# Kernel optimization log

Measured on AMD Instinct MI355X. Metric: run time of the kernel, lower is better.

The kernel has to match this reference:

```python
import jax, jax.numpy as jnp
import numpy as np

D = 128          # embed_features
N = 4096         # cells per batch
M = 8192         # genes / regions
FB1, FB2, FR, FA = 100, 100, 256, 512


def setup_inputs() -> dict:
    key = jax.random.key(0)
    ks = jax.random.split(key, 16)
    s = 0.05  # weight scale to keep activations in a sane range
    return {
        "u1": jax.random.normal(ks[0], (N, FB1), jnp.float32),
        "u2": jax.random.normal(ks[1], (N, FB2), jnp.float32),
        "v1": jax.random.normal(ks[2], (M, FR), jnp.float32),
        "v2": jax.random.normal(ks[3], (M, FA), jnp.float32),
        # linear layers stored as [in, out] so y = x @ W
        "Wb1": jax.random.normal(ks[4], (FB1, D), jnp.float32) * s,
        "Wb2": jax.random.normal(ks[5], (FB2, D), jnp.float32) * s,
        "Wrna1": jax.random.normal(ks[6], (FR, 2 * D), jnp.float32) * s,
        "Wrna2": jax.random.normal(ks[7], (2 * D, D), jnp.float32) * s,
        "gene_act": jax.random.normal(ks[8], (FA, FR), jnp.float32) * s,
        "w_prod1": jax.random.normal(ks[9], (D,), jnp.float32),
        "w_add1": jax.random.normal(ks[10], (2 * D,), jnp.float32),
        "w_prod2": jax.random.normal(ks[11], (D,), jnp.float32),
        "w_add2": jax.random.normal(ks[12], (2 * D,), jnp.float32),
        "bias_1": jax.random.normal(ks[13], (), jnp.float32),
        "bias_2": jax.random.normal(ks[14], (), jnp.float32),
    }


def _pair_scores(eu, ev, w_prod, w_add, bias):
    # Algebraically identical to the original all-pairs form:
    #   (eu[:,None,:] * ev[None,:,:]) @ w_prod  ==  (eu * w_prod) @ ev.T
    #   cat(eu, ev) @ w_add  ==  eu @ w_add[:D]  +  ev @ w_add[D:]
    prod = (eu * w_prod) @ ev.T                     # [N, M]
    add = (eu @ w_add[:D])[:, None] + (ev @ w_add[D:])[None, :]
    return prod + add + bias                        # [N, M]


def reference(u1, u2, v1, v2, Wb1, Wb2, Wrna1, Wrna2, gene_act,
              w_prod1, w_add1, w_prod2, w_add2, bias_1, bias_2):
    # mode='linear' activations -> identity
    embed_u1 = u1 @ Wb1                                          # [N, D]
    embed_v1 = jax.nn.relu(v1 @ Wrna1) @ Wrna2                   # [M, D]
    out1 = jax.nn.relu(_pair_scores(embed_u1, embed_v1, w_prod1, w_add1, bias_1))

    embed_u2 = u2 @ Wb2                                          # [N, D]
    embed_v2 = jax.nn.relu((v2 @ gene_act) @ Wrna1) @ Wrna2      # [M, D]
    out2 = jax.nn.sigmoid(_pair_scores(embed_u2, embed_v2, w_prod2, w_add2, bias_2))

    return out1, out2, embed_u1, embed_v1, embed_u2, embed_v2
```

## Files before the change

### kernel.cpp

```cpp
#include <hip/hip_runtime.h>
#include <math.h>

#define N_CELLS 4096
#define M_GENES 8192

typedef __attribute__((ext_vector_type(8))) short short8;
typedef __attribute__((ext_vector_type(4))) float f32x4;

__device__ __align__(16) float g_a[24576];

__device__ __align__(16) short g_bu1[N_CELLS * 128];
__device__ __align__(16) short g_bv1[M_GENES * 128];
__device__ __align__(16) short g_bu2[N_CELLS * 128];
__device__ __align__(16) short g_bv2[M_GENES * 128];

__device__ __align__(16) short g_gaT[256 * 512];
__device__ __align__(16) short g_W1T[256 * 256];
__device__ __align__(16) short g_W2T[128 * 256];


__device__ __forceinline__ short* bf_sel(int s) {
    switch (s) {
        case 0:  return g_bu1;
        case 1:  return g_bv1;
        case 2:  return g_bu2;
        default: return g_bv2;
    }
}

__device__ __forceinline__ const short* wt_sel(int s) {
    switch (s) {
        case 0:  return g_gaT;
        case 1:  return g_W1T;
        default: return g_W2T;
    }
}

__device__ __forceinline__ short f2bf(float f) {
    unsigned u = __builtin_bit_cast(unsigned, f);
    u += 0x7FFFu + ((u >> 16) & 1u);
    return (short)(u >> 16);
}

__device__ __forceinline__ void cvt8(const float* __restrict__ in, short* __restrict__ out) {
    const float4 x0 = *reinterpret_cast<const float4*>(in);
    const float4 x1 = *reinterpret_cast<const float4*>(in + 4);
    short8 o;
    o[0] = f2bf(x0.x); o[1] = f2bf(x0.y); o[2] = f2bf(x0.z); o[3] = f2bf(x0.w);
    o[4] = f2bf(x1.x); o[5] = f2bf(x1.y); o[6] = f2bf(x1.z); o[7] = f2bf(x1.w);
    *reinterpret_cast<short8*>(out) = o;
}

__device__ __forceinline__ void transpose8(const float* __restrict__ in, short* __restrict__ out,
                                           int c, int K, int Nc) {
    const int o0 = c * 8;
    const int ncol = o0 / K;
    const int k0 = o0 % K;
    short8 o;
#pragma unroll
    for (int j = 0; j < 8; ++j) o[j] = f2bf(in[(size_t)(k0 + j) * Nc + ncol]);
    *reinterpret_cast<short8*>(out + o0) = o;
}

__device__ __forceinline__ void stage_A_f32(char* cA, const float* Af, int row0, int k0, int K, int t)
{
    const float* gAf = Af + (size_t)row0 * K + k0;
#pragma unroll
    for (int c = 0; c < 4; ++c) {
        const int idx = c * 256 + t;
        const int row = idx >> 4, sub = idx & 15;
        const int dst = row * 256 + ((sub * 16) ^ ((row & 7) << 4));
        cvt8(gAf + (size_t)row * K + sub * 8, (short*)(cA + dst));
    }
}

__device__ __forceinline__ void stage_B128(char* cB, const short* BT, int col0, int k0, int K, int t)
{
    const char* gB = (const char*)(BT + (size_t)col0 * K + k0);
#pragma unroll
    for (int c = 0; c < 8; ++c) {
        const int idx = c * 256 + t;
        const int row = idx >> 4, sub = idx & 15;
        const int dst = row * 256 + ((sub * 16) ^ ((row & 7) << 4));
        *(short8*)(cB + dst) = *(const short8*)(gB + (size_t)row * (2 * K) + sub * 16);
    }
}

__device__ __forceinline__ void stage_B64(char* cB, const short* BT, int col0, int k0, int K, int t)
{
    const char* gB = (const char*)(BT + (size_t)col0 * K + k0);
#pragma unroll
    for (int c = 0; c < 4; ++c) {
        const int idx = c * 256 + t;
        const int row = idx >> 4, sub = idx & 15;
        const int dst = row * 256 + ((sub * 16) ^ ((row & 7) << 4));
        *(short8*)(cB + dst) = *(const short8*)(gB + (size_t)row * (2 * K) + sub * 16);
    }
}

__device__ __forceinline__ void mfma128(const char* cA, int strideA, int baseA,
                                        const char* cB, f32x4 (&acc)[2][4], int t)
{
    const int l = t & 63, w = t >> 6;
    const int wm = (w >> 1) * 32, wn = (w & 1) * 64;
    const int lr = l & 15, lkb = (l >> 4) * 16;
#pragma unroll
    for (int kk = 0; kk < 4; ++kk) {
        const int kb = kk * 64 + lkb;
        short8 a[2], b4[4];
#pragma unroll
        for (int i = 0; i < 2; ++i) {
            const int rA = wm + i * 16 + lr;
            a[i] = *(const short8*)(cA + rA * strideA + ((baseA + kb) ^ ((rA & 7) << 4)));
        }
#pragma unroll
        for (int jj = 0; jj < 4; ++jj) {
            const int rB = wn + jj * 16 + lr;
            b4[jj] = *(const short8*)(cB + rB * 256 + (kb ^ ((rB & 7) << 4)));
        }
#pragma unroll
        for (int i = 0; i < 2; ++i)
#pragma unroll
            for (int jj = 0; jj < 4; ++jj)
                acc[i][jj] = __builtin_amdgcn_mfma_f32_16x16x32_bf16(a[i], b4[jj], acc[i][jj], 0, 0, 0);
    }
}

__device__ __forceinline__ void mfma64(const char* cA, int strideA, int baseA,
                                       const char* cB, f32x4 (&acc)[4], int t)
{
    const int l = t & 63, w = t >> 6;
    const int wm = w * 16;
    const int lr = l & 15, lkb = (l >> 4) * 16;
#pragma unroll
    for (int kk = 0; kk < 4; ++kk) {
        const int kb = kk * 64 + lkb;
        const int rA = wm + lr;
        const short8 a = *(const short8*)(cA + rA * strideA + ((baseA + kb) ^ ((rA & 7) << 4)));
#pragma unroll
        for (int jj = 0; jj < 4; ++jj) {
            const int rB = jj * 16 + lr;
            const short8 b = *(const short8*)(cB + rB * 256 + (kb ^ ((rB & 7) << 4)));
            acc[jj] = __builtin_amdgcn_mfma_f32_16x16x32_bf16(a, b, acc[jj], 0, 0, 0);
        }
    }
}

__device__ __forceinline__ void acc_to_sH(char* sH, const f32x4 (&acc)[2][4], int ct, bool relu, int t)
{
    const int l = t & 63, w = t >> 6;
    const int wm = (w >> 1) * 32, wn = (w & 1) * 64;
    const int lr = l & 15, r4 = (l >> 4) * 4;
#pragma unroll
    for (int i = 0; i < 2; ++i)
#pragma unroll
        for (int r = 0; r < 4; ++r) {
            const int row = wm + i * 16 + r4 + r;
#pragma unroll
            for (int jj = 0; jj < 4; ++jj) {
                float x = acc[i][jj][r];
                if (relu) x = fmaxf(x, 0.f);
                const int col = ct * 128 + wn + jj * 16 + lr;
                *(short*)(sH + row * 512 + ((col * 2) ^ ((row & 7) << 4))) = f2bf(x);
            }
        }
}

__device__ __forceinline__ void acc2_to_sH(char* sH, const f32x4 (&a4)[4], int ct, bool relu, int t)
{
    const int l = t & 63, w = t >> 6;
    const int lr = l & 15, r4 = (l >> 4) * 4;
#pragma unroll
    for (int r = 0; r < 4; ++r) {
        const int row = w * 16 + r4 + r;
#pragma unroll
        for (int jj = 0; jj < 4; ++jj) {
            float x = a4[jj][r];
            if (relu) x = fmaxf(x, 0.f);
            const int col = ct * 64 + jj * 16 + lr;
            *(short*)(sH + row * 512 + ((col * 2) ^ ((row & 7) << 4))) = f2bf(x);
        }
    }
}

__device__ __forceinline__ void first_layer(const float* Vf, int row0, int KV, int bsel, bool relu,
                                            char* cA, char* cH, int t)
{
    const short* BT = wt_sel(bsel);
    f32x4 accA[2][4] = {}, accB[2][4] = {};
    for (int k0 = 0; k0 < KV; k0 += 128) {
        stage_A_f32(cA, Vf, row0, k0, KV, t);
        stage_B128(cH, BT, 0, k0, KV, t);
        __syncthreads();
        mfma128(cA, 256, 0, cH, accA, t);
        __syncthreads();
        stage_B128(cH, BT, 128, k0, KV, t);
        __syncthreads();
        mfma128(cA, 256, 0, cH, accB, t);
        __syncthreads();
    }
    acc_to_sH(cH, accA, 0, relu, t);
    acc_to_sH(cH, accB, 1, relu, t);
    __syncthreads();
}

__device__ __forceinline__ void mid_layer(char* cH, char* cB64, int t)
{
    const short* W1T = wt_sel(1);
    f32x4 h4[4][4];
#pragma unroll
    for (int ct = 0; ct < 4; ++ct)
#pragma unroll
        for (int jj = 0; jj < 4; ++jj) h4[ct][jj] = (f32x4){0.f, 0.f, 0.f, 0.f};
#pragma unroll
    for (int ct = 0; ct < 4; ++ct)
        for (int k0 = 0; k0 < 2; ++k0) {
            stage_B64(cB64, W1T, ct * 64, k0 * 128, 256, t);
            __syncthreads();
            mfma64(cH, 512, k0 * 256, cB64, h4[ct], t);
            __syncthreads();
        }
#pragma unroll
    for (int ct = 0; ct < 4; ++ct) acc2_to_sH(cH, h4[ct], ct, true, t);
    __syncthreads();
}

__device__ __forceinline__ void final_layer(char* cH, char* cB64, float* evout, short* bv,
                                            const float* w_add_hi, int a_ofs, int row0, int t)
{
    const short* W2T = wt_sel(2);
    const int l = t & 63, w = t >> 6, lr = l & 15, r4 = (l >> 4) * 4;
    float part[4] = {0.f, 0.f, 0.f, 0.f};
#pragma unroll
    for (int ct = 0; ct < 2; ++ct) {
        f32x4 a2[4] = {};
        for (int k0 = 0; k0 < 2; ++k0) {
            stage_B64(cB64, W2T, ct * 64, k0 * 128, 256, t);
            __syncthreads();
            mfma64(cH, 512, k0 * 256, cB64, a2, t);
            __syncthreads();
        }
#pragma unroll
        for (int r = 0; r < 4; ++r) {
            const int grow = row0 + w * 16 + r4 + r;
#pragma unroll
            for (int jj = 0; jj < 4; ++jj) {
                const float x = a2[jj][r];
                const int col = ct * 64 + jj * 16 + lr;
                evout[(size_t)grow * 128 + col] = x;
                bv[(size_t)grow * 128 + col] = f2bf(x);
                part[r] = fmaf(x, w_add_hi[col], part[r]);
            }
        }
    }
#pragma unroll
    for (int off = 1; off < 16; off <<= 1)
#pragma unroll
        for (int r = 0; r < 4; ++r) part[r] += __shfl_xor(part[r], off, 64);
    if (lr == 0) {
#pragma unroll
        for (int r = 0; r < 4; ++r) g_a[a_ofs + row0 + w * 16 + r4 + r] = part[r];
    }
}

__device__ __forceinline__ void embed8(int be, const float* u1, const float* u2,
        const float* Wb1, const float* Wb2, const float* wp1, const float* wa1,
        const float* wp2, const float* wa2, float* eu1, float* eu2, float* sMemF)
{
    const int which = (be >= 512) ? 1 : 0;
    const int bl = which ? (be - 512) : be;
    const float* u  = which ? u2 : u1;
    const float* Wb = which ? Wb2 : Wb1;
    const float* wp = which ? wp2 : wp1;
    const float* wa = which ? wa2 : wa1;
    float* e  = which ? eu2 : eu1;
    short* bu = bf_sel(which ? 2 : 0);
    const int a_ofs = which ? 12288 : 0;
    const int row0 = bl * 8;
    float* sWb = sMemF;
    float* sUu = sMemF + 12800;
    float* sF  = sMemF + 13600;
    const int t = threadIdx.x;
    for (int c = t; c < 3200; c += 256)
        ((float4*)sWb)[c] = ((const float4*)Wb)[c];
    for (int c = t; c < 800; c += 256) sUu[c] = u[row0 * 100 + c];
    if (t < 8) sF[t] = 0.f;
    __syncthreads();
    const int d = t & 127, g = t >> 7;
    float acc[4] = {0.f, 0.f, 0.f, 0.f};
    for (int k = 0; k < 100; ++k) {
        const float wv = sWb[k * 128 + d];
#pragma unroll
        for (int rr = 0; rr < 4; ++rr) acc[rr] = fmaf(wv, sUu[(g * 4 + rr) * 100 + k], acc[rr]);
    }
    const float wpd = wp[d], wad = wa[d];
    float pv[4];
#pragma unroll
    for (int rr = 0; rr < 4; ++rr) {
        const int row = row0 + g * 4 + rr;
        e[(size_t)row * 128 + d] = acc[rr];
        bu[(size_t)row * 128 + d] = f2bf(acc[rr] * wpd);
        pv[rr] = acc[rr] * wad;
    }
#pragma unroll
    for (int off = 32; off > 0; off >>= 1)
#pragma unroll
        for (int rr = 0; rr < 4; ++rr) pv[rr] += __shfl_down(pv[rr], off, 64);
    if ((t & 63) == 0) {
#pragma unroll
        for (int rr = 0; rr < 4; ++rr) atomicAdd(&sF[g * 4 + rr], pv[rr]);
    }
    __syncthreads();
    if (t < 8) g_a[a_ofs + row0 + t] = sF[t];
}

__global__ __launch_bounds__(256) void prep_w(const float* __restrict__ gene_act,
                                              const float* __restrict__ W1,
                                              const float* __restrict__ W2)
{
    const int b = blockIdx.x, t = threadIdx.x;
    if (b < 64)      transpose8(gene_act, g_gaT, b * 256 + t, 512, 256);
    else if (b < 96) transpose8(W1, g_W1T, (b - 64) * 256 + t, 256, 256);
    else             transpose8(W2, g_W2T, (b - 96) * 256 + t, 256, 128);
}

__global__ __launch_bounds__(256) void fused_mid(const float* __restrict__ v1,
                                                 const float* __restrict__ v2,
                                                 const float* __restrict__ u1,
                                                 const float* __restrict__ u2,
                                                 const float* __restrict__ Wb1,
                                                 const float* __restrict__ Wb2,
                                                 const float* __restrict__ wp1,
                                                 const float* __restrict__ wa1,
                                                 const float* __restrict__ wp2,
                                                 const float* __restrict__ wa2,
                                                 float* __restrict__ eu1,
                                                 float* __restrict__ eu2,
                                                 float* __restrict__ ev1,
                                                 float* __restrict__ ev2)
{
    __shared__ __align__(16) short sMem[32768];
    char* cA   = (char*)sMem;
    char* cB64 = cA + 16384;
    char* cH   = cA + 32768;
    const int b = blockIdx.x, t = threadIdx.x;
    if (b < 128) {
        const int row0 = b * 64;
        first_layer(v2, row0, 512, 0, false, cA, cH, t);
        mid_layer(cH, cB64, t);
        final_layer(cH, cB64, ev2, bf_sel(3), wa2 + 128, 16384, row0, t);
    } else if (b < 256) {
        const int row0 = (b - 128) * 64;
        first_layer(v1, row0, 256, 1, true, cA, cH, t);
        final_layer(cH, cB64, ev1, bf_sel(1), wa1 + 128, 4096, row0, t);
    } else {
        embed8(b - 256, u1, u2, Wb1, Wb2, wp1, wa1, wp2, wa2, eu1, eu2, (float*)sMem);
    }
}

__global__ __launch_bounds__(256) void pair_both(const float* __restrict__ bias1,
                                                 const float* __restrict__ bias2,
                                                 float* __restrict__ out1,
                                                 float* __restrict__ out2)
{
    __shared__ __align__(16) short sA[128 * 128];
    __shared__ __align__(16) short sB[128 * 128];
    const int which = blockIdx.z;
    const int t = threadIdx.x;
    const int l = t & 63;
    const int row0 = blockIdx.y * 128;
    const int col0 = blockIdx.x * 128;

    {
        const short8* gA = reinterpret_cast<const short8*>(bf_sel(which ? 2 : 0)) + (size_t)row0 * 16;
        const short8* gB = reinterpret_cast<const short8*>(bf_sel(which ? 3 : 1)) + (size_t)col0 * 16;
        char* cA = (char*)sA;
        char* cB = (char*)sB;
#pragma unroll
        for (int c = 0; c < 8; ++c) {
            const int idx = c * 256 + t;
            const int row = idx >> 4, sub = idx & 15;
            const int dst = row * 256 + ((sub * 16) ^ ((row & 7) << 4));
            const short8 va = gA[idx];
            const short8 vb = gB[idx];
            *(short8*)(cA + dst) = va;
            *(short8*)(cB + dst) = vb;
        }
    }
    __syncthreads();

    const int w  = t >> 6;
    const int wm = (w >> 1) * 64;
    const int wn = (w & 1) * 64;
    const int lr = l & 15;
    const int lkb = (l >> 4) * 16;

    f32x4 acc[4][4] = {};
    const char* cA = (const char*)sA;
    const char* cB = (const char*)sB;
#pragma unroll
    for (int kk = 0; kk < 4; ++kk) {
        const int kb = kk * 64 + lkb;
        short8 a[4], bfr[4];
#pragma unroll
        for (int i = 0; i < 4; ++i) {
            const int rowA = wm + i * 16 + lr;
            a[i] = *(const short8*)(cA + rowA * 256 + (kb ^ ((rowA & 7) << 4)));
            const int rowB = wn + i * 16 + lr;
            bfr[i] = *(const short8*)(cB + rowB * 256 + (kb ^ ((rowB & 7) << 4)));
        }
#pragma unroll
        for (int i = 0; i < 4; ++i)
#pragma unroll
            for (int jj = 0; jj < 4; ++jj)
                acc[i][jj] = __builtin_amdgcn_mfma_f32_16x16x32_bf16(a[i], bfr[jj], acc[i][jj], 0, 0, 0);
    }

    const float bias = which ? *bias2 : *bias1;
    float* outp = which ? out2 : out1;
    const int ofsU = which ? 12288 : 0;
    const int ofsV = which ? 16384 : 4096;
    const int r4 = (l >> 4) * 4;
    float au[4][4];
#pragma unroll
    for (int i = 0; i < 4; ++i)
#pragma unroll
        for (int r = 0; r < 4; ++r)
            au[i][r] = g_a[ofsU + row0 + wm + i * 16 + r4 + r];
    float av[4];
#pragma unroll
    for (int jj = 0; jj < 4; ++jj)
        av[jj] = g_a[ofsV + col0 + wn + jj * 16 + lr];

#pragma unroll
    for (int i = 0; i < 4; ++i) {
#pragma unroll
        for (int r = 0; r < 4; ++r) {
            const int grow = row0 + wm + i * 16 + r4 + r;
            float* orow = outp + (size_t)grow * M_GENES + col0 + wn;
#pragma unroll
            for (int jj = 0; jj < 4; ++jj) {
                float x = acc[i][jj][r] + au[i][r] + av[jj] + bias;
                if (which == 0) x = fmaxf(x, 0.f);
                else            x = __builtin_amdgcn_rcpf(1.f + __expf(-x));
                orow[jj * 16 + lr] = x;
            }
        }
    }
}

extern "C" void kernel_launch(void* const* d_in, const int* in_sizes, int n_in,
                              void* d_out, int out_size, void* d_ws, size_t ws_size,
                              hipStream_t stream)
{
    const float* u1       = (const float*)d_in[0];
    const float* u2       = (const float*)d_in[1];
    const float* v1       = (const float*)d_in[2];
    const float* v2       = (const float*)d_in[3];
    const float* Wb1      = (const float*)d_in[4];
    const float* Wb2      = (const float*)d_in[5];
    const float* Wrna1    = (const float*)d_in[6];
    const float* Wrna2    = (const float*)d_in[7];
    const float* gene_act = (const float*)d_in[8];
    const float* w_prod1  = (const float*)d_in[9];
    const float* w_add1   = (const float*)d_in[10];
    const float* w_prod2  = (const float*)d_in[11];
    const float* w_add2   = (const float*)d_in[12];
    const float* bias1    = (const float*)d_in[13];
    const float* bias2    = (const float*)d_in[14];

    float* out  = (float*)d_out;
    float* out1 = out;
    float* out2 = out1 + (size_t)N_CELLS * M_GENES;
    float* eu1  = out2 + (size_t)N_CELLS * M_GENES;
    float* ev1  = eu1 + N_CELLS * 128;
    float* eu2  = ev1 + M_GENES * 128;
    float* ev2  = eu2 + N_CELLS * 128;

    prep_w<<<112, 256, 0, stream>>>(gene_act, Wrna1, Wrna2);

    fused_mid<<<1280, 256, 0, stream>>>(v1, v2, u1, u2, Wb1, Wb2,
                                        w_prod1, w_add1, w_prod2, w_add2,
                                        eu1, eu2, ev1, ev2);

    pair_both<<<dim3(64, 32, 2), 256, 0, stream>>>(bias1, bias2, out1, out2);
}
```

Baseline: 114.7 us.

## Stage pair-score outputs through LDS for coalesced float4 stores, use 512 threads

The pair kernel now runs 512 threads per block with 8 waves each computing a 64x32 sub-tile, which halves the per-wave accumulators and raises wave count. The output tile is written into reused shared memory with an XOR swizzle and then streamed to global memory as contiguous float4 rows. Previously each lane stored scattered 4-byte values. The goal is better coalescing of the large output write, which dominates this memory-bound kernel, at the cost of two extra barriers and an LDS round trip.

Measured after the change: 126.6 us. +10.4%, slower.

```diff
diff --git a/kernel.cpp b/kernel.cpp
--- a/kernel.cpp
+++ b/kernel.cpp
@@ -358,13 +358,14 @@
     }
 }
 
-__global__ __launch_bounds__(256) void pair_both(const float* __restrict__ bias1,
-                                                 const float* __restrict__ bias2,
-                                                 float* __restrict__ out1,
-                                                 float* __restrict__ out2)
-{
-    __shared__ __align__(16) short sA[128 * 128];
-    __shared__ __align__(16) short sB[128 * 128];
+__global__ __launch_bounds__(512, 4) void pair_both(const float* __restrict__ bias1,
+                                                    const float* __restrict__ bias2,
+                                                    float* __restrict__ out1,
+                                                    float* __restrict__ out2)
+{
+    __shared__ __align__(16) short sMem[32768];
+    char* cU = (char*)sMem;
+    char* cV = cU + 32768;
     const int which = blockIdx.z;
     const int t = threadIdx.x;
     const int l = t & 63;
@@ -374,50 +375,49 @@
     {
         const short8* gA = reinterpret_cast<const short8*>(bf_sel(which ? 2 : 0)) + (size_t)row0 * 16;
         const short8* gB = reinterpret_cast<const short8*>(bf_sel(which ? 3 : 1)) + (size_t)col0 * 16;
-        char* cA = (char*)sA;
-        char* cB = (char*)sB;
-#pragma unroll
-        for (int c = 0; c < 8; ++c) {
-            const int idx = c * 256 + t;
+#pragma unroll
+        for (int c = 0; c < 4; ++c) {
+            const int idx = c * 512 + t;
             const int row = idx >> 4, sub = idx & 15;
             const int dst = row * 256 + ((sub * 16) ^ ((row & 7) << 4));
             const short8 va = gA[idx];
             const short8 vb = gB[idx];
-            *(short8*)(cA + dst) = va;
-            *(short8*)(cB + dst) = vb;
+            *(short8*)(cU + dst) = va;
+            *(short8*)(cV + dst) = vb;
         }
     }
     __syncthreads();
 
     const int w  = t >> 6;
-    const int wm = (w >> 1) * 64;
-    const int wn = (w & 1) * 64;
+    const int wm = (w >> 2) * 64;
+    const int wn = (w & 3) * 32;
     const int lr = l & 15;
     const int lkb = (l >> 4) * 16;
 
-    f32x4 acc[4][4] = {};
-    const char* cA = (const char*)sA;
-    const char* cB = (const char*)sB;
+    f32x4 acc[4][2] = {};
 #pragma unroll
     for (int kk = 0; kk < 4; ++kk) {
         const int kb = kk * 64 + lkb;
-        short8 a[4], bfr[4];
+        short8 a[4], b2[2];
 #pragma unroll
         for (int i = 0; i < 4; ++i) {
-            const int rowA = wm + i * 16 + lr;
-            a[i] = *(const short8*)(cA + rowA * 256 + (kb ^ ((rowA & 7) << 4)));
-            const int rowB = wn + i * 16 + lr;
-            bfr[i] = *(const short8*)(cB + rowB * 256 + (kb ^ ((rowB & 7) << 4)));
+            const int rA = wm + i * 16 + lr;
+            a[i] = *(const short8*)(cU + rA * 256 + (kb ^ ((rA & 7) << 4)));
+        }
+#pragma unroll
+        for (int j = 0; j < 2; ++j) {
+            const int rB = wn + j * 16 + lr;
+            b2[j] = *(const short8*)(cV + rB * 256 + (kb ^ ((rB & 7) << 4)));
         }
 #pragma unroll
         for (int i = 0; i < 4; ++i)
 #pragma unroll
-            for (int jj = 0; jj < 4; ++jj)
-                acc[i][jj] = __builtin_amdgcn_mfma_f32_16x16x32_bf16(a[i], bfr[jj], acc[i][jj], 0, 0, 0);
-    }
+            for (int j = 0; j < 2; ++j)
+                acc[i][j] = __builtin_amdgcn_mfma_f32_16x16x32_bf16(a[i], b2[j], acc[i][j], 0, 0, 0);
+    }
+    __syncthreads();
 
     const float bias = which ? *bias2 : *bias1;
-    float* outp = which ? out2 : out1;
     const int ofsU = which ? 12288 : 0;
     const int ofsV = which ? 16384 : 4096;
     const int r4 = (l >> 4) * 4;
@@ -427,24 +427,40 @@
 #pragma unroll
         for (int r = 0; r < 4; ++r)
             au[i][r] = g_a[ofsU + row0 + wm + i * 16 + r4 + r];
-    float av[4];
-#pragma unroll
-    for (int jj = 0; jj < 4; ++jj)
-        av[jj] = g_a[ofsV + col0 + wn + jj * 16 + lr];
-
+    float av[2];
+#pragma unroll
+    for (int j = 0; j < 2; ++j)
+        av[j] = g_a[ofsV + col0 + wn + j * 16 + lr];
+
+    char* cF = (char*)sMem;
 #pragma unroll
     for (int i = 0; i < 4; ++i) {
 #pragma unroll
         for (int r = 0; r < 4; ++r) {
-            const int grow = row0 + wm + i * 16 + r4 + r;
-            float* orow = outp + (size_t)grow * M_GENES + col0 + wn;
-#pragma unroll
-            for (int jj = 0; jj < 4; ++jj) {
-                float x = acc[i][jj][r] + au[i][r] + av[jj] + bias;
+            const int row = wm + i * 16 + r4 + r;
+#pragma unroll
+            for (int j = 0; j < 2; ++j) {
+                float x = acc[i][j][r] + au[i][r] + av[j] + bias;
                 if (which == 0) x = fmaxf(x, 0.f);
                 else            x = __builtin_amdgcn_rcpf(1.f + __expf(-x));
-                orow[jj * 16 + lr] = x;
+                const int col = wn + j * 16 + lr;
+                *(float*)(cF + row * 512 + ((col * 4) ^ ((row & 7) << 4))) = x;
             }
+        }
+    }
+    __syncthreads();
+
+    float* outp = which ? out2 : out1;
+#pragma unroll
+    for (int p = 0; p < 2; ++p) {
+        const int row = p * 64 + (t >> 3);
+        const char* base = cF + row * 512;
+        float* grow = outp + (size_t)(row0 + row) * M_GENES + col0;
+#pragma unroll
+        for (int q = 0; q < 4; ++q) {
+            const int c4 = (t & 7) + q * 8;
+            const float4 v = *(const float4*)(base + ((c4 * 16) ^ ((row & 7) << 4)));
+            *reinterpret_cast<float4*>(grow + c4 * 4) = v;
         }
     }
 }
@@ -483,5 +499,5 @@
                                         w_prod1, w_add1, w_prod2, w_add2,
                                         eu1, eu2, ev1, ev2);
 
-    pair_both<<<dim3(64, 32, 2), 256, 0, stream>>>(bias1, bias2, out1, out2);
-}
+    pair_both<<<dim3(64, 32, 2), 512, 0, stream>>>(bias1, bias2, out1, out2);
+}
```

## Compute cell embeddings with bf16 MFMA and pre-convert inputs in prep kernel

Applied to the files above, without the earlier changes.

Replaces the scalar FP32 embed8 path (1024 blocks computing 8 rows each) with 128 blocks that each compute 64 rows of u@Wb using bf16 MFMA tiles. u1/u2 are converted to padded bf16 and Wb transposed to bf16 in the prep kernel. This moves cell-embedding arithmetic onto matrix cores and shrinks the fused_mid grid. In exchange it adds an extra pass over u in prep, and the eu outputs are now computed from bf16 inputs, lowering their precision.

Measured after the change: 115.9 us. No clear change (+1.1%).

```diff
diff --git a/kernel.cpp b/kernel.cpp
--- a/kernel.cpp
+++ b/kernel.cpp
@@ -17,6 +17,10 @@
 __device__ __align__(16) short g_gaT[256 * 512];
 __device__ __align__(16) short g_W1T[256 * 256];
 __device__ __align__(16) short g_W2T[128 * 256];
+__device__ __align__(16) short g_ub1[N_CELLS * 128];
+__device__ __align__(16) short g_ub2[N_CELLS * 128];
+__device__ __align__(16) short g_WbT1[128 * 128];
+__device__ __align__(16) short g_WbT2[128 * 128];
 
 
 __device__ __forceinline__ short* bf_sel(int s) {
@@ -263,73 +267,51 @@
     }
 }
 
-__device__ __forceinline__ void embed8(int be, const float* u1, const float* u2,
-        const float* Wb1, const float* Wb2, const float* wp1, const float* wa1,
-        const float* wp2, const float* wa2, float* eu1, float* eu2, float* sMemF)
-{
-    const int which = (be >= 512) ? 1 : 0;
-    const int bl = which ? (be - 512) : be;
-    const float* u  = which ? u2 : u1;
-    const float* Wb = which ? Wb2 : Wb1;
-    const float* wp = which ? wp2 : wp1;
-    const float* wa = which ? wa2 : wa1;
-    float* e  = which ? eu2 : eu1;
-    short* bu = bf_sel(which ? 2 : 0);
-    const int a_ofs = which ? 12288 : 0;
-    const int row0 = bl * 8;
-    float* sWb = sMemF;
-    float* sUu = sMemF + 12800;
-    float* sF  = sMemF + 13600;
-    const int t = threadIdx.x;
-    for (int c = t; c < 3200; c += 256)
-        ((float4*)sWb)[c] = ((const float4*)Wb)[c];
-    for (int c = t; c < 800; c += 256) sUu[c] = u[row0 * 100 + c];
-    if (t < 8) sF[t] = 0.f;
-    __syncthreads();
-    const int d = t & 127, g = t >> 7;
-    float acc[4] = {0.f, 0.f, 0.f, 0.f};
-    for (int k = 0; k < 100; ++k) {
-        const float wv = sWb[k * 128 + d];
-#pragma unroll
-        for (int rr = 0; rr < 4; ++rr) acc[rr] = fmaf(wv, sUu[(g * 4 + rr) * 100 + k], acc[rr]);
-    }
-    const float wpd = wp[d], wad = wa[d];
-    float pv[4];
-#pragma unroll
-    for (int rr = 0; rr < 4; ++rr) {
-        const int row = row0 + g * 4 + rr;
-        e[(size_t)row * 128 + d] = acc[rr];
-        bu[(size_t)row * 128 + d] = f2bf(acc[rr] * wpd);
-        pv[rr] = acc[rr] * wad;
-    }
-#pragma unroll
-    for (int off = 32; off > 0; off >>= 1)
-#pragma unroll
-        for (int rr = 0; rr < 4; ++rr) pv[rr] += __shfl_down(pv[rr], off, 64);
-    if ((t & 63) == 0) {
-#pragma unroll
-        for (int rr = 0; rr < 4; ++rr) atomicAdd(&sF[g * 4 + rr], pv[rr]);
-    }
-    __syncthreads();
-    if (t < 8) g_a[a_ofs + row0 + t] = sF[t];
-}
-
-__global__ __launch_bounds__(256) void prep_w(const float* __restrict__ gene_act,
-                                              const float* __restrict__ W1,
-                                              const float* __restrict__ W2)
-{
-    const int b = blockIdx.x, t = threadIdx.x;
-    if (b < 64)      transpose8(gene_act, g_gaT, b * 256 + t, 512, 256);
-    else if (b < 96) transpose8(W1, g_W1T, (b - 64) * 256 + t, 256, 256);
-    else             transpose8(W2, g_W2T, (b - 96) * 256 + t, 256, 128);
-}
-
-__global__ __launch_bounds__(256) void fused_mid(const float* __restrict__ v1,
-                                                 const float* __restrict__ v2,
+__global__ __launch_bounds__(256) void prep_all2(const float* __restrict__ gene_act,
+                                                 const float* __restrict__ W1,
+                                                 const float* __restrict__ W2,
                                                  const float* __restrict__ u1,
                                                  const float* __restrict__ u2,
                                                  const float* __restrict__ Wb1,
-                                                 const float* __restrict__ Wb2,
+                                                 const float* __restrict__ Wb2)
+{
+    const int b = blockIdx.x, t = threadIdx.x;
+    if (b < 64)       transpose8(gene_act, g_gaT, b * 256 + t, 512, 256);
+    else if (b < 96)  transpose8(W1, g_W1T, (b - 64) * 256 + t, 256, 256);
+    else if (b < 112) transpose8(W2, g_W2T, (b - 96) * 256 + t, 256, 128);
+    else if (b < 624) {
+        const int which = (b >= 368);
+        const int c = (b - (which ? 368 : 112)) * 256 + t;
+        const float* u = which ? u2 : u1;
+        short* ub = which ? g_ub2 : g_ub1;
+        const int row = c >> 4, sub = c & 15;
+        short8 o = {0, 0, 0, 0, 0, 0, 0, 0};
+        if (sub < 12) {
+            const float4 x0 = *(const float4*)(u + row * 100 + sub * 8);
+            const float4 x1 = *(const float4*)(u + row * 100 + sub * 8 + 4);
+            o[0] = f2bf(x0.x); o[1] = f2bf(x0.y); o[2] = f2bf(x0.z); o[3] = f2bf(x0.w);
+            o[4] = f2bf(x1.x); o[5] = f2bf(x1.y); o[6] = f2bf(x1.z); o[7] = f2bf(x1.w);
+        } else if (sub == 12) {
+            const float4 x0 = *(const float4*)(u + row * 100 + 96);
+            o[0] = f2bf(x0.x); o[1] = f2bf(x0.y); o[2] = f2bf(x0.z); o[3] = f2bf(x0.w);
+        }
+        *(short8*)(ub + (size_t)c * 8) = o;
+    } else {
+        const int which = (b >= 632);
+        const int c = (b - (which ? 632 : 624)) * 256 + t;
+        const float* Wb = which ? Wb2 : Wb1;
+        short* wt = which ? g_WbT2 : g_WbT1;
+        const int col = c >> 4, k0 = (c & 15) * 8;
+        short8 o;
+#pragma unroll
+        for (int j = 0; j < 8; ++j)
+            o[j] = (k0 + j < 100) ? f2bf(Wb[(size_t)(k0 + j) * 128 + col]) : (short)0;
+        *(short8*)(wt + (size_t)c * 8) = o;
+    }
+}
+
+__global__ __launch_bounds__(256) void fused_mid(const float* __restrict__ v1,
+                                                 const float* __restrict__ v2,
                                                  const float* __restrict__ wp1,
                                                  const float* __restrict__ wa1,
                                                  const float* __restrict__ wp2,
@@ -354,7 +336,68 @@
         first_layer(v1, row0, 256, 1, true, cA, cH, t);
         final_layer(cH, cB64, ev1, bf_sel(1), wa1 + 128, 4096, row0, t);
     } else {
-        embed8(b - 256, u1, u2, Wb1, Wb2, wp1, wa1, wp2, wa2, eu1, eu2, (float*)sMem);
+        const int eb = b - 256;
+        const int which = eb >> 6;
+        const int row0 = (eb & 63) * 64;
+        const short* Au  = which ? g_ub2  : g_ub1;
+        const short* WbT = which ? g_WbT2 : g_WbT1;
+        const float* wp = which ? wp2 : wp1;
+        const float* wa = which ? wa2 : wa1;
+        float* eu = which ? eu2 : eu1;
+        short* bu = bf_sel(which ? 2 : 0);
+        const int a_ofs = which ? 12288 : 0;
+
+        stage_B64(cA, Au, row0, 0, 128, t);
+        stage_B128(cH, WbT, 0, 0, 128, t);
+        __syncthreads();
+        f32x4 acc[2][4] = {};
+        mfma128(cA, 256, 0, cH, acc, t);
+        __syncthreads();
+
+        const int l = t & 63, w = t >> 6;
+        const int wm = (w >> 1) * 32, wn = (w & 1) * 64;
+        const int lr = l & 15, r4 = (l >> 4) * 4;
+        float* sRow = (float*)cB64;
+        float wvp[4], wva[4];
+#pragma unroll
+        for (int jj = 0; jj < 4; ++jj) {
+            const int col = wn + jj * 16 + lr;
+            wvp[jj] = wp[col];
+            wva[jj] = wa[col];
+        }
+        float part[2][4] = {};
+#pragma unroll
+        for (int i = 0; i < 2; ++i)
+#pragma unroll
+            for (int r = 0; r < 4; ++r) {
+                const int grow = row0 + wm + i * 16 + r4 + r;
+#pragma unroll
+                for (int jj = 0; jj < 4; ++jj) {
+                    const float x = acc[i][jj][r];
+                    const int col = wn + jj * 16 + lr;
+                    eu[(size_t)grow * 128 + col] = x;
+                    bu[(size_t)grow * 128 + col] = f2bf(x * wvp[jj]);
+                    part[i][r] = fmaf(x, wva[jj], part[i][r]);
+                }
+            }
+#pragma unroll
+        for (int off = 1; off < 16; off <<= 1)
+#pragma unroll
+            for (int i = 0; i < 2; ++i)
+#pragma unroll
+                for (int r = 0; r < 4; ++r)
+                    part[i][r] += __shfl_xor(part[i][r], off, 64);
+        if (t < 64) sRow[t] = 0.f;
+        __syncthreads();
+        if (lr == 0) {
+#pragma unroll
+            for (int i = 0; i < 2; ++i)
+#pragma unroll
+                for (int r = 0; r < 4; ++r)
+                    atomicAdd(&sRow[wm + i * 16 + r4 + r], part[i][r]);
+        }
+        __syncthreads();
+        if (t < 64) g_a[a_ofs + row0 + t] = sRow[t];
     }
 }
 
@@ -477,11 +520,10 @@
     float* eu2  = ev1 + M_GENES * 128;
     float* ev2  = eu2 + N_CELLS * 128;
 
-    prep_w<<<112, 256, 0, stream>>>(gene_act, Wrna1, Wrna2);
-
-    fused_mid<<<1280, 256, 0, stream>>>(v1, v2, u1, u2, Wb1, Wb2,
-                                        w_prod1, w_add1, w_prod2, w_add2,
-                                        eu1, eu2, ev1, ev2);
+    prep_all2<<<640, 256, 0, stream>>>(gene_act, Wrna1, Wrna2, u1, u2, Wb1, Wb2);
+
+    fused_mid<<<384, 256, 0, stream>>>(v1, v2, w_prod1, w_add1, w_prod2, w_add2,
+                                       eu1, eu2, ev1, ev2);
 
     pair_both<<<dim3(64, 32, 2), 256, 0, stream>>>(bias1, bias2, out1, out2);
 }
```
